# Optimization experiments

Hardware: AMD Instinct MI355X
Metric: run time of the kernel (lower is better)

The kernel has to match this reference:

```python
import jax, jax.numpy as jnp
import numpy as np
from jax import lax

KSIZE = 7


def _box_sum(x, k):
    # x: [B,1,Hp,Wp] already reflect-padded; valid kxk sliding-window sum
    return lax.reduce_window(x, 0.0, lax.add, (1, 1, k, k), (1, 1, 1, 1), 'VALID')


def _local_var(residual, k):
    # Unbiased sliding-window variance via box filter (sum / sum-of-squares),
    # equivalent to torch unfold + var(dim=(-1,-2), unbiased=True).
    pad = (k - 1) // 2
    rp = jnp.pad(residual, ((0, 0), (0, 0), (pad, pad), (pad, pad)), mode='reflect')
    n = float(k * k)
    s = _box_sum(rp, k)
    ss = _box_sum(rp * rp, k)
    return (ss - s * s / n) / (n - 1.0)


def setup_inputs() -> dict:
    key = jax.random.key(0)
    k1, k2, k3 = jax.random.split(key, 3)
    shape = (16, 3, 512, 512)
    return {
        'output': jax.random.normal(k1, shape, dtype=jnp.float32),
        'output_ema': jax.random.normal(k2, shape, dtype=jnp.float32),
        'gt': jax.random.normal(k3, shape, dtype=jnp.float32),
    }


def reference(output, output_ema, gt):
    # residuals summed over channels, keepdim -> [B,1,H,W]
    residual_ema = jnp.sum(jnp.abs(gt - output_ema), axis=1, keepdims=True)
    residual_sr = jnp.sum(jnp.abs(gt - output), axis=1, keepdims=True)
    # global (per-image) unbiased variance over (C,H,W), keepdims -> [B,1,1,1]
    patch_level_weight = jnp.var(residual_sr, axis=(1, 2, 3), keepdims=True, ddof=1) ** 0.2
    # local 7x7 unbiased variance -> [B,1,H,W]
    pixel_level_weight = _local_var(residual_sr, KSIZE)
    overall_weight = patch_level_weight * pixel_level_weight
    overall_weight = jnp.where(residual_sr < residual_ema, 0.0, overall_weight)
    # L1 criterion on weighted images (weight broadcasts over channels)
    return jnp.mean(jnp.abs(overall_weight * output - overall_weight * gt))
```

## Files before the change

kernel.cpp:

```cpp
#include <hip/hip_runtime.h>
#include <math.h>

#define BB 16
#define CC 3
#define HH 512
#define WW 512
#define HW (HH*WW)
#define TOTAL ((double)(BB*CC*HW))

#define TSTR 76


__global__ __launch_bounds__(256, 5) void k_main(
    const float* __restrict__ outp, const float* __restrict__ emap,
    const float* __restrict__ gtp,
    double* __restrict__ ps, double* __restrict__ pss, double* __restrict__ pl)
{
    __shared__ float tile[70 * TSTR];
    __shared__ double red[12];

    const int t  = threadIdx.x;
    const int bx = blockIdx.x, by = blockIdx.y, b = blockIdx.z;
    const int x0 = bx * 64 - 3, y0 = by * 64 - 3;

    const size_t ib = (size_t)b * (CC * HW);
    const float4* o4 = (const float4*)(outp + ib);
    const float4* e4 = (const float4*)(emap + ib);
    const float4* g4 = (const float4*)(gtp + ib);

    double s_loc = 0.0, ss_loc = 0.0;

    for (int iter = 0; iter < 4; ++iter) {
        int i   = iter * 256 + t;
        int row = i >> 4;
        int fc  = i & 15;
        int idx = (by * 64 + row) * (WW / 4) + (bx * 16 + fc);
        float4 rs = {0.f, 0.f, 0.f, 0.f};
        float4 re = {0.f, 0.f, 0.f, 0.f};
#pragma unroll
        for (int c = 0; c < CC; ++c) {
            float4 g = g4[c * (HW / 4) + idx];
            float4 o = o4[c * (HW / 4) + idx];
            float4 e = e4[c * (HW / 4) + idx];
            rs.x += fabsf(g.x - o.x); rs.y += fabsf(g.y - o.y);
            rs.z += fabsf(g.z - o.z); rs.w += fabsf(g.w - o.w);
            re.x += fabsf(g.x - e.x); re.y += fabsf(g.y - e.y);
            re.z += fabsf(g.z - e.z); re.w += fabsf(g.w - e.w);
        }
        float4 enc;
        enc.x = (rs.x < re.x) ? -rs.x : rs.x;
        enc.y = (rs.y < re.y) ? -rs.y : rs.y;
        enc.z = (rs.z < re.z) ? -rs.z : rs.z;
        enc.w = (rs.w < re.w) ? -rs.w : rs.w;
        *(float4*)&tile[(row + 3) * TSTR + 4 + fc * 4] = enc;

        s_loc  += (double)rs.x + (double)rs.y + (double)rs.z + (double)rs.w;
        ss_loc += (double)rs.x * rs.x + (double)rs.y * rs.y +
                  (double)rs.z * rs.z + (double)rs.w * rs.w;
    }

    for (int i = t; i < 804; i += 256) {
        int ly, lx;
        if (i < 210)      { ly = i / 70;                lx = i % 70; }
        else if (i < 420) { int j = i - 210; ly = 67 + j / 70;  lx = j % 70; }
        else if (i < 612) { int j = i - 420; ly = 3 + (j & 63); lx = j >> 6; }
        else              { int j = i - 612; ly = 3 + (j & 63); lx = 67 + (j >> 6); }
        int gy = y0 + ly; gy = gy < 0 ? -gy : (gy >= HH ? 2 * HH - 2 - gy : gy);
        int gx = x0 + lx; gx = gx < 0 ? -gx : (gx >= WW ? 2 * WW - 2 - gx : gx);
        size_t idx = ib + (size_t)(gy * WW + gx);
        float r = 0.f;
#pragma unroll
        for (int c = 0; c < CC; ++c) {
            float g = gtp[idx + c * HW];
            float o = outp[idx + c * HW];
            r += fabsf(g - o);
        }
        tile[ly * TSTR + 1 + lx] = r;
    }
    __syncthreads();

    const int x  = t & 63;
    const int w  = t >> 6;
    const int r0 = w * 16;

    float rS[7], rSS[7];
    float winS = 0.f, winSS = 0.f;
#pragma unroll
    for (int j = 0; j < 7; ++j) {
        float S = 0.f, SS = 0.f;
#pragma unroll
        for (int dx = 0; dx < 7; ++dx) {
            float v = tile[(r0 + j) * TSTR + x + 1 + dx];
            S += fabsf(v);
            SS = fmaf(v, v, SS);
        }
        rS[j] = S; rSS[j] = SS;
        winS += S; winSS += SS;
    }
    double acc = 0.0;
#pragma unroll
    for (int k = 0; k < 16; ++k) {
        if (k) {
            const int slot = (k - 1) % 7;
            float S = 0.f, SS = 0.f;
#pragma unroll
            for (int dx = 0; dx < 7; ++dx) {
                float v = tile[(r0 + k + 6) * TSTR + x + 1 + dx];
                S += fabsf(v);
                SS = fmaf(v, v, SS);
            }
            winS  += S  - rS[slot];
            winSS += SS - rSS[slot];
            rS[slot] = S; rSS[slot] = SS;
        }
        float cen = tile[(r0 + k + 3) * TSTR + x + 4];
        float rr  = fabsf(cen);
        float pvar = (winSS - winS * winS * (1.0f / 49.0f)) * (1.0f / 48.0f);
        float contrib = (__float_as_uint(cen) >> 31) ? 0.0f : fabsf(pvar) * rr;
        acc += (double)contrib;
    }

    for (int off = 32; off; off >>= 1) {
        s_loc  += __shfl_down(s_loc, off);
        ss_loc += __shfl_down(ss_loc, off);
        acc    += __shfl_down(acc, off);
    }
    if ((t & 63) == 0) { red[w] = s_loc; red[4 + w] = ss_loc; red[8 + w] = acc; }
    __syncthreads();
    if (t == 0) {
        int bid = b * 64 + by * 8 + bx;
        ps[bid]  = red[0] + red[1] + red[2] + red[3];
        pss[bid] = red[4] + red[5] + red[6] + red[7];
        pl[bid]  = red[8] + red[9] + red[10] + red[11];
    }
}

__global__ __launch_bounds__(256) void k_final(
    const double* __restrict__ ps, const double* __restrict__ pss,
    const double* __restrict__ pl, float* __restrict__ out)
{
    const int t = threadIdx.x, lane = t & 63, w = t >> 6;
    __shared__ double wacc[4];
    double tot = 0.0;
    for (int m = 0; m < 4; ++m) {
        int b = w * 4 + m;
        double s  = ps[b * 64 + lane];
        double ss = pss[b * 64 + lane];
        double L  = pl[b * 64 + lane];
        for (int off = 32; off; off >>= 1) {
            s  += __shfl_down(s, off);
            ss += __shfl_down(ss, off);
            L  += __shfl_down(L, off);
        }
        if (lane == 0) {
            double n = (double)HW;
            double var = (ss - s * s / n) / (n - 1.0);
            tot += (double)powf((float)var, 0.2f) * L;
        }
    }
    if (lane == 0) wacc[w] = tot;
    __syncthreads();
    if (t == 0) out[0] = (float)((wacc[0] + wacc[1] + wacc[2] + wacc[3]) / TOTAL);
}

extern "C" void kernel_launch(void* const* d_in, const int* in_sizes, int n_in,
                              void* d_out, int out_size, void* d_ws, size_t ws_size,
                              hipStream_t stream)
{
    const float* outp = (const float*)d_in[0];
    const float* emap = (const float*)d_in[1];
    const float* gtp  = (const float*)d_in[2];

    char* ws = (char*)d_ws;
    double* ps  = (double*)(ws);
    double* pss = (double*)(ws + 8192);
    double* pl  = (double*)(ws + 16384);

    k_main<<<dim3(8, 8, BB), 256, 0, stream>>>(outp, emap, gtp, ps, pss, pl);
    k_final<<<1, 256, 0, stream>>>(ps, pss, pl, (float*)d_out);
}
```

Baseline: 176.2 us.

## Split fused kernel into residual-map pass and row-band local-variance pass

Replaces the single tiled kernel, which recomputed halo residuals from all three inputs, with two kernels. The first writes a signed residual map to workspace and accumulates global sums. The second reads full-width 8-row bands of that map and computes the 7x7 local variance. This removes the costly scattered halo reloads of gt and output, at the cost of an extra 16 MB write plus its read-back and one more kernel launch.

```diff
diff --git a/kernel.cpp b/kernel.cpp
--- a/kernel.cpp
+++ b/kernel.cpp
@@ -6,42 +6,34 @@
 #define HH 512
 #define WW 512
 #define HW (HH*WW)
+#define PLANE4 (HW/4)
 #define TOTAL ((double)(BB*CC*HW))
 
-#define TSTR 76
 
-
-__global__ __launch_bounds__(256, 5) void k_main(
-    const float* __restrict__ outp, const float* __restrict__ emap,
-    const float* __restrict__ gtp,
-    double* __restrict__ ps, double* __restrict__ pss, double* __restrict__ pl)
+__global__ __launch_bounds__(256, 4) void k_resid(
+    const float4* __restrict__ o4, const float4* __restrict__ e4,
+    const float4* __restrict__ g4, float4* __restrict__ rsr4,
+    double* __restrict__ ps, double* __restrict__ pss)
 {
-    __shared__ float tile[70 * TSTR];
-    __shared__ double red[12];
-
-    const int t  = threadIdx.x;
-    const int bx = blockIdx.x, by = blockIdx.y, b = blockIdx.z;
-    const int x0 = bx * 64 - 3, y0 = by * 64 - 3;
-
-    const size_t ib = (size_t)b * (CC * HW);
-    const float4* o4 = (const float4*)(outp + ib);
-    const float4* e4 = (const float4*)(emap + ib);
-    const float4* g4 = (const float4*)(gtp + ib);
+    const int t   = threadIdx.x;
+    const int blk = blockIdx.x;
+    const int img = blk >> 6;
+    const int sub = blk & 63;
+    const size_t ib = (size_t)img * (CC * PLANE4);
+    const size_t rb = (size_t)img * PLANE4;
+    const int p0 = sub * 1024 + t;
 
     double s_loc = 0.0, ss_loc = 0.0;
-
-    for (int iter = 0; iter < 4; ++iter) {
-        int i   = iter * 256 + t;
-        int row = i >> 4;
-        int fc  = i & 15;
-        int idx = (by * 64 + row) * (WW / 4) + (bx * 16 + fc);
+#pragma unroll
+    for (int pp = 0; pp < 4; ++pp) {
+        const int p = p0 + pp * 256;
         float4 rs = {0.f, 0.f, 0.f, 0.f};
         float4 re = {0.f, 0.f, 0.f, 0.f};
 #pragma unroll
         for (int c = 0; c < CC; ++c) {
-            float4 g = g4[c * (HW / 4) + idx];
-            float4 o = o4[c * (HW / 4) + idx];
-            float4 e = e4[c * (HW / 4) + idx];
+            float4 g = g4[ib + c * PLANE4 + p];
+            float4 o = o4[ib + c * PLANE4 + p];
+            float4 e = e4[ib + c * PLANE4 + p];
             rs.x += fabsf(g.x - o.x); rs.y += fabsf(g.y - o.y);
             rs.z += fabsf(g.z - o.z); rs.w += fabsf(g.w - o.w);
             re.x += fabsf(g.x - e.x); re.y += fabsf(g.y - e.y);
@@ -52,87 +44,106 @@
         enc.y = (rs.y < re.y) ? -rs.y : rs.y;
         enc.z = (rs.z < re.z) ? -rs.z : rs.z;
         enc.w = (rs.w < re.w) ? -rs.w : rs.w;
-        *(float4*)&tile[(row + 3) * TSTR + 4 + fc * 4] = enc;
+        rsr4[rb + p] = enc;
 
         s_loc  += (double)rs.x + (double)rs.y + (double)rs.z + (double)rs.w;
         ss_loc += (double)rs.x * rs.x + (double)rs.y * rs.y +
                   (double)rs.z * rs.z + (double)rs.w * rs.w;
     }
 
-    for (int i = t; i < 804; i += 256) {
-        int ly, lx;
-        if (i < 210)      { ly = i / 70;                lx = i % 70; }
-        else if (i < 420) { int j = i - 210; ly = 67 + j / 70;  lx = j % 70; }
-        else if (i < 612) { int j = i - 420; ly = 3 + (j & 63); lx = j >> 6; }
-        else              { int j = i - 612; ly = 3 + (j & 63); lx = 67 + (j >> 6); }
-        int gy = y0 + ly; gy = gy < 0 ? -gy : (gy >= HH ? 2 * HH - 2 - gy : gy);
-        int gx = x0 + lx; gx = gx < 0 ? -gx : (gx >= WW ? 2 * WW - 2 - gx : gx);
-        size_t idx = ib + (size_t)(gy * WW + gx);
-        float r = 0.f;
+    for (int off = 32; off; off >>= 1) {
+        s_loc  += __shfl_down(s_loc, off);
+        ss_loc += __shfl_down(ss_loc, off);
+    }
+    __shared__ double red[8];
+    const int wid = t >> 6;
+    if ((t & 63) == 0) { red[wid] = s_loc; red[4 + wid] = ss_loc; }
+    __syncthreads();
+    if (t == 0) {
+        ps[blk]  = red[0] + red[1] + red[2] + red[3];
+        pss[blk] = red[4] + red[5] + red[6] + red[7];
+    }
+}
+
+#define TST 520
+__global__ __launch_bounds__(256, 4) void k_band(
+    const float* __restrict__ rsr, double* __restrict__ pl)
+{
+    __shared__ float tile[14 * TST];
+    __shared__ double red[4];
+    const int t   = threadIdx.x;
+    const int bx  = blockIdx.x;
+    const int img = blockIdx.y;
+    const int r0  = bx * 8;
+    const float*  rp  = rsr + (size_t)img * HW;
+    const float4* rp4 = (const float4*)rp;
+
 #pragma unroll
-        for (int c = 0; c < CC; ++c) {
-            float g = gtp[idx + c * HW];
-            float o = outp[idx + c * HW];
-            r += fabsf(g - o);
-        }
-        tile[ly * TSTR + 1 + lx] = r;
+    for (int it = 0; it < 7; ++it) {
+        int idx = it * 256 + t;
+        int lr  = idx >> 7, c4 = idx & 127;
+        int gr  = r0 - 3 + lr;
+        gr = gr < 0 ? -gr : (gr > HH - 1 ? 2 * HH - 2 - gr : gr);
+        *(float4*)&tile[lr * TST + 4 + c4 * 4] = rp4[gr * (WW / 4) + c4];
+    }
+    if (t < 84) {
+        int lr = t / 6, j = t % 6;
+        int gr = r0 - 3 + lr;
+        gr = gr < 0 ? -gr : (gr > HH - 1 ? 2 * HH - 2 - gr : gr);
+        int dst, gx;
+        if (j < 3) { dst = 1 + j;        gx = 3 - j;   }
+        else       { int jr = j - 3; dst = 516 + jr; gx = 510 - jr; }
+        tile[lr * TST + dst] = rp[gr * WW + gx];
     }
     __syncthreads();
 
-    const int x  = t & 63;
-    const int w  = t >> 6;
-    const int r0 = w * 16;
-
-    float rS[7], rSS[7];
-    float winS = 0.f, winSS = 0.f;
+    double accL = 0.0;
 #pragma unroll
-    for (int j = 0; j < 7; ++j) {
-        float S = 0.f, SS = 0.f;
+    for (int cc = 0; cc < 2; ++cc) {
+        const int x  = t + cc * 256;
+        const int cb = x + 1;
+        float rS[7], rSS[7];
+        float winS = 0.f, winSS = 0.f;
 #pragma unroll
-        for (int dx = 0; dx < 7; ++dx) {
-            float v = tile[(r0 + j) * TSTR + x + 1 + dx];
-            S += fabsf(v);
-            SS = fmaf(v, v, SS);
-        }
-        rS[j] = S; rSS[j] = SS;
-        winS += S; winSS += SS;
-    }
-    double acc = 0.0;
-#pragma unroll
-    for (int k = 0; k < 16; ++k) {
-        if (k) {
-            const int slot = (k - 1) % 7;
+        for (int j = 0; j < 7; ++j) {
             float S = 0.f, SS = 0.f;
 #pragma unroll
             for (int dx = 0; dx < 7; ++dx) {
-                float v = tile[(r0 + k + 6) * TSTR + x + 1 + dx];
+                float v = tile[j * TST + cb + dx];
                 S += fabsf(v);
                 SS = fmaf(v, v, SS);
             }
-            winS  += S  - rS[slot];
-            winSS += SS - rSS[slot];
-            rS[slot] = S; rSS[slot] = SS;
+            rS[j] = S; rSS[j] = SS;
+            winS += S; winSS += SS;
         }
-        float cen = tile[(r0 + k + 3) * TSTR + x + 4];
-        float rr  = fabsf(cen);
-        float pvar = (winSS - winS * winS * (1.0f / 49.0f)) * (1.0f / 48.0f);
-        float contrib = (__float_as_uint(cen) >> 31) ? 0.0f : fabsf(pvar) * rr;
-        acc += (double)contrib;
+#pragma unroll
+        for (int k = 0; k < 8; ++k) {
+            if (k) {
+                const int slot = k - 1;
+                float S = 0.f, SS = 0.f;
+#pragma unroll
+                for (int dx = 0; dx < 7; ++dx) {
+                    float v = tile[(k + 6) * TST + cb + dx];
+                    S += fabsf(v);
+                    SS = fmaf(v, v, SS);
+                }
+                winS  += S  - rS[slot];
+                winSS += SS - rSS[slot];
+                rS[slot] = S; rSS[slot] = SS;
+            }
+            float cen = tile[(k + 3) * TST + x + 4];
+            float rr  = fabsf(cen);
+            float pvar = (winSS - winS * winS * (1.0f / 49.0f)) * (1.0f / 48.0f);
+            float contrib = (__float_as_uint(cen) >> 31) ? 0.0f : fabsf(pvar) * rr;
+            accL += (double)contrib;
+        }
     }
 
-    for (int off = 32; off; off >>= 1) {
-        s_loc  += __shfl_down(s_loc, off);
-        ss_loc += __shfl_down(ss_loc, off);
-        acc    += __shfl_down(acc, off);
-    }
-    if ((t & 63) == 0) { red[w] = s_loc; red[4 + w] = ss_loc; red[8 + w] = acc; }
+    for (int off = 32; off; off >>= 1) accL += __shfl_down(accL, off);
+    const int wid = t >> 6;
+    if ((t & 63) == 0) red[wid] = accL;
     __syncthreads();
-    if (t == 0) {
-        int bid = b * 64 + by * 8 + bx;
-        ps[bid]  = red[0] + red[1] + red[2] + red[3];
-        pss[bid] = red[4] + red[5] + red[6] + red[7];
-        pl[bid]  = red[8] + red[9] + red[10] + red[11];
-    }
+    if (t == 0) pl[img * 64 + bx] = red[0] + red[1] + red[2] + red[3];
 }
 
 __global__ __launch_bounds__(256) void k_final(
@@ -167,15 +178,18 @@
                               void* d_out, int out_size, void* d_ws, size_t ws_size,
                               hipStream_t stream)
 {
-    const float* outp = (const float*)d_in[0];
-    const float* emap = (const float*)d_in[1];
-    const float* gtp  = (const float*)d_in[2];
+    const float4* o4 = (const float4*)d_in[0];
+    const float4* e4 = (const float4*)d_in[1];
+    const float4* g4 = (const float4*)d_in[2];
 
     char* ws = (char*)d_ws;
-    double* ps  = (double*)(ws);
-    double* pss = (double*)(ws + 8192);
-    double* pl  = (double*)(ws + 16384);
+    float4* rsr4 = (float4*)(ws);
+    float*  rsr  = (float*)(ws);
+    double* ps   = (double*)(ws + 16777216);
+    double* pss  = (double*)(ws + 16785408);
+    double* pl   = (double*)(ws + 16793600);
 
-    k_main<<<dim3(8, 8, BB), 256, 0, stream>>>(outp, emap, gtp, ps, pss, pl);
+    k_resid<<<1024, 256, 0, stream>>>(o4, e4, g4, rsr4, ps, pss);
+    k_band<<<dim3(64, BB), 256, 0, stream>>>(rsr, pl);
     k_final<<<1, 256, 0, stream>>>(ps, pss, pl, (float*)d_out);
 }
```

New measurement: 181.6 us. 1.03x slower.

## Shrink tiles to 64x32 and load halo with unified vectorized float4 path

Applied to the files above, without the earlier changes.

Halves the tile height from 64 to 32 rows, which doubles the grid to 2048 blocks and shrinks shared memory per block. The interior and most of the halo are now loaded together in one float4 loop; only the left and right edge columns that need reflection fall back to scalar loads. The aim is more parallelism and coalesced halo loads instead of scattered scalar loads. In exchange, the halo overhead per tile rises (38 rows loaded for 32 output rows), and the final reduction reads twice as many partial sums.

```diff
diff --git a/kernel.cpp b/kernel.cpp
--- a/kernel.cpp
+++ b/kernel.cpp
@@ -6,82 +6,91 @@
 #define HH 512
 #define WW 512
 #define HW (HH*WW)
+#define PLANE4 (HW/4)
+#define W4 (WW/4)
 #define TOTAL ((double)(BB*CC*HW))
 
-#define TSTR 76
+typedef float f32x4 __attribute__((ext_vector_type(4)));
+
+#define TSTR 72
 
 
-__global__ __launch_bounds__(256, 5) void k_main(
-    const float* __restrict__ outp, const float* __restrict__ emap,
-    const float* __restrict__ gtp,
+__global__ __launch_bounds__(256, 4) void k_main(
+    const f32x4* __restrict__ o4, const f32x4* __restrict__ e4,
+    const f32x4* __restrict__ g4,
     double* __restrict__ ps, double* __restrict__ pss, double* __restrict__ pl)
 {
-    __shared__ float tile[70 * TSTR];
+    __shared__ float tile[38 * TSTR];
     __shared__ double red[12];
 
     const int t  = threadIdx.x;
-    const int bx = blockIdx.x, by = blockIdx.y, b = blockIdx.z;
-    const int x0 = bx * 64 - 3, y0 = by * 64 - 3;
-
-    const size_t ib = (size_t)b * (CC * HW);
-    const float4* o4 = (const float4*)(outp + ib);
-    const float4* e4 = (const float4*)(emap + ib);
-    const float4* g4 = (const float4*)(gtp + ib);
+    const int bx = blockIdx.x;
+    const int by = blockIdx.y;
+    const int b  = blockIdx.z;
+    const int y0 = by * 32;
+    const size_t ib = (size_t)b * (CC * PLANE4);
 
     double s_loc = 0.0, ss_loc = 0.0;
 
-    for (int iter = 0; iter < 4; ++iter) {
-        int i   = iter * 256 + t;
-        int row = i >> 4;
-        int fc  = i & 15;
-        int idx = (by * 64 + row) * (WW / 4) + (bx * 16 + fc);
-        float4 rs = {0.f, 0.f, 0.f, 0.f};
-        float4 re = {0.f, 0.f, 0.f, 0.f};
+    for (int i = t; i < 38 * 18; i += 256) {
+        const int lr = i / 18;
+        const int lc = i - lr * 18;
+        int gy = y0 - 3 + lr;
+        gy = gy < 0 ? -gy : (gy > HH - 1 ? 2 * HH - 2 - gy : gy);
+        const int gx4 = bx * 16 - 1 + lc;
+        const bool interior = (lr >= 3) & (lr < 35) & (lc >= 1) & (lc < 17);
+
+        if (gx4 >= 0 && gx4 < W4) {
+            const size_t idx = ib + (size_t)gy * W4 + gx4;
+            f32x4 g0 = g4[idx];
+            f32x4 g1 = g4[idx + PLANE4];
+            f32x4 g2 = g4[idx + 2 * PLANE4];
+            f32x4 q0 = o4[idx];
+            f32x4 q1 = o4[idx + PLANE4];
+            f32x4 q2 = o4[idx + 2 * PLANE4];
+            f32x4 rsv;
 #pragma unroll
-        for (int c = 0; c < CC; ++c) {
-            float4 g = g4[c * (HW / 4) + idx];
-            float4 o = o4[c * (HW / 4) + idx];
-            float4 e = e4[c * (HW / 4) + idx];
-            rs.x += fabsf(g.x - o.x); rs.y += fabsf(g.y - o.y);
-            rs.z += fabsf(g.z - o.z); rs.w += fabsf(g.w - o.w);
-            re.x += fabsf(g.x - e.x); re.y += fabsf(g.y - e.y);
-            re.z += fabsf(g.z - e.z); re.w += fabsf(g.w - e.w);
+            for (int j = 0; j < 4; ++j)
+                rsv[j] = fabsf(g0[j] - q0[j]) + fabsf(g1[j] - q1[j]) + fabsf(g2[j] - q2[j]);
+
+            if (interior) {
+                f32x4 e0 = e4[idx];
+                f32x4 e1 = e4[idx + PLANE4];
+                f32x4 e2 = e4[idx + 2 * PLANE4];
+                f32x4 enc;
+#pragma unroll
+                for (int j = 0; j < 4; ++j) {
+                    float re = fabsf(g0[j] - e0[j]) + fabsf(g1[j] - e1[j]) + fabsf(g2[j] - e2[j]);
+                    float rs = rsv[j];
+                    enc[j] = (rs < re) ? -rs : rs;
+                    s_loc  += (double)rs;
+                    ss_loc += (double)rs * rs;
+                }
+                *(f32x4*)&tile[lr * TSTR + lc * 4] = enc;
+            } else {
+                *(f32x4*)&tile[lr * TSTR + lc * 4] = rsv;
+            }
+        } else {
+            const float* gp = (const float*)g4;
+            const float* op = (const float*)o4;
+#pragma unroll
+            for (int j = 0; j < 4; ++j) {
+                int gx = gx4 * 4 + j;
+                gx = gx < 0 ? -gx : (gx > WW - 1 ? 2 * WW - 2 - gx : gx);
+                const size_t idx = ib * 4 + (size_t)gy * WW + gx;
+                float r = 0.f;
+#pragma unroll
+                for (int c = 0; c < CC; ++c)
+                    r += fabsf(gp[idx + c * HW] - op[idx + c * HW]);
+                tile[lr * TSTR + lc * 4 + j] = r;
+            }
         }
-        float4 enc;
-        enc.x = (rs.x < re.x) ? -rs.x : rs.x;
-        enc.y = (rs.y < re.y) ? -rs.y : rs.y;
-        enc.z = (rs.z < re.z) ? -rs.z : rs.z;
-        enc.w = (rs.w < re.w) ? -rs.w : rs.w;
-        *(float4*)&tile[(row + 3) * TSTR + 4 + fc * 4] = enc;
-
-        s_loc  += (double)rs.x + (double)rs.y + (double)rs.z + (double)rs.w;
-        ss_loc += (double)rs.x * rs.x + (double)rs.y * rs.y +
-                  (double)rs.z * rs.z + (double)rs.w * rs.w;
-    }
-
-    for (int i = t; i < 804; i += 256) {
-        int ly, lx;
-        if (i < 210)      { ly = i / 70;                lx = i % 70; }
-        else if (i < 420) { int j = i - 210; ly = 67 + j / 70;  lx = j % 70; }
-        else if (i < 612) { int j = i - 420; ly = 3 + (j & 63); lx = j >> 6; }
-        else              { int j = i - 612; ly = 3 + (j & 63); lx = 67 + (j >> 6); }
-        int gy = y0 + ly; gy = gy < 0 ? -gy : (gy >= HH ? 2 * HH - 2 - gy : gy);
-        int gx = x0 + lx; gx = gx < 0 ? -gx : (gx >= WW ? 2 * WW - 2 - gx : gx);
-        size_t idx = ib + (size_t)(gy * WW + gx);
-        float r = 0.f;
-#pragma unroll
-        for (int c = 0; c < CC; ++c) {
-            float g = gtp[idx + c * HW];
-            float o = outp[idx + c * HW];
-            r += fabsf(g - o);
-        }
-        tile[ly * TSTR + 1 + lx] = r;
     }
     __syncthreads();
 
     const int x  = t & 63;
     const int w  = t >> 6;
-    const int r0 = w * 16;
+    const int r0 = w * 8;
 
     float rS[7], rSS[7];
     float winS = 0.f, winSS = 0.f;
@@ -99,9 +108,9 @@
     }
     double acc = 0.0;
 #pragma unroll
-    for (int k = 0; k < 16; ++k) {
+    for (int k = 0; k < 8; ++k) {
         if (k) {
-            const int slot = (k - 1) % 7;
+            const int slot = k - 1;
             float S = 0.f, SS = 0.f;
 #pragma unroll
             for (int dx = 0; dx < 7; ++dx) {
@@ -125,10 +134,11 @@
         ss_loc += __shfl_down(ss_loc, off);
         acc    += __shfl_down(acc, off);
     }
-    if ((t & 63) == 0) { red[w] = s_loc; red[4 + w] = ss_loc; red[8 + w] = acc; }
+    const int wid = t >> 6;
+    if ((t & 63) == 0) { red[wid] = s_loc; red[4 + wid] = ss_loc; red[8 + wid] = acc; }
     __syncthreads();
     if (t == 0) {
-        int bid = b * 64 + by * 8 + bx;
+        const int bid = (b * 16 + by) * 8 + bx;
         ps[bid]  = red[0] + red[1] + red[2] + red[3];
         pss[bid] = red[4] + red[5] + red[6] + red[7];
         pl[bid]  = red[8] + red[9] + red[10] + red[11];
@@ -144,9 +154,9 @@
     double tot = 0.0;
     for (int m = 0; m < 4; ++m) {
         int b = w * 4 + m;
-        double s  = ps[b * 64 + lane];
-        double ss = pss[b * 64 + lane];
-        double L  = pl[b * 64 + lane];
+        double s  = ps[b * 128 + lane] + ps[b * 128 + 64 + lane];
+        double ss = pss[b * 128 + lane] + pss[b * 128 + 64 + lane];
+        double L  = pl[b * 128 + lane] + pl[b * 128 + 64 + lane];
         for (int off = 32; off; off >>= 1) {
             s  += __shfl_down(s, off);
             ss += __shfl_down(ss, off);
@@ -167,15 +177,15 @@
                               void* d_out, int out_size, void* d_ws, size_t ws_size,
                               hipStream_t stream)
 {
-    const float* outp = (const float*)d_in[0];
-    const float* emap = (const float*)d_in[1];
-    const float* gtp  = (const float*)d_in[2];
+    const f32x4* o4 = (const f32x4*)d_in[0];
+    const f32x4* e4 = (const f32x4*)d_in[1];
+    const f32x4* g4 = (const f32x4*)d_in[2];
 
     char* ws = (char*)d_ws;
     double* ps  = (double*)(ws);
-    double* pss = (double*)(ws + 8192);
-    double* pl  = (double*)(ws + 16384);
+    double* pss = (double*)(ws + 16384);
+    double* pl  = (double*)(ws + 32768);
 
-    k_main<<<dim3(8, 8, BB), 256, 0, stream>>>(outp, emap, gtp, ps, pss, pl);
+    k_main<<<dim3(8, 16, BB), 256, 0, stream>>>(o4, e4, g4, ps, pss, pl);
     k_final<<<1, 256, 0, stream>>>(ps, pss, pl, (float*)d_out);
 }
```

Result: faster. 169.1 us (-4.0%).
